# Kernel tuning notes

Measured on AMD Instinct MI355X. Metric: run time of the kernel, lower is better.

The kernel has to match this reference:

```python
import jax, jax.numpy as jnp
import numpy as np

N_NODES = 10000
N_EDGES = 320000
N_GRAPHS = 64


def _gcn_conv(x, edge_index, W, b, n):
    # PyG GCNConv: add self-loops, symmetric deg^-1/2 normalization, x@W, scatter-add at target, + bias
    loop = jnp.arange(n)
    src = jnp.concatenate([edge_index[0], loop])
    dst = jnp.concatenate([edge_index[1], loop])
    deg = jax.ops.segment_sum(jnp.ones_like(dst, dtype=x.dtype), dst, num_segments=n)
    dinv = jnp.where(deg > 0, 1.0 / jnp.sqrt(jnp.maximum(deg, 1.0)), 0.0)
    norm = dinv[src] * dinv[dst]            # [E']
    h = x @ W                               # [N, out]
    out = jax.ops.segment_sum(h[src] * norm[:, None], dst, num_segments=n)
    return out + b


def _mean_pool(x, batch, g):
    s = jax.ops.segment_sum(x, batch, num_segments=g)
    cnt = jax.ops.segment_sum(jnp.ones((x.shape[0],), x.dtype), batch, num_segments=g)
    return s / jnp.maximum(cnt, 1.0)[:, None]


def setup_inputs() -> dict:
    key = jax.random.key(0)
    ks = jax.random.split(key, 20)
    x = jax.random.normal(ks[0], (N_NODES, 1), dtype=jnp.float32)
    edge_index = jax.random.randint(ks[1], (2, N_EDGES), 0, N_NODES, dtype=jnp.int64)
    batch = jnp.sort(jax.random.randint(ks[2], (N_NODES,), 0, N_GRAPHS, dtype=jnp.int64))

    def lin(k, fi, fo):
        k1, k2 = jax.random.split(k)
        lim = 1.0 / np.sqrt(fi)
        W = jax.random.uniform(k1, (fi, fo), jnp.float32, -lim, lim)
        b = jax.random.uniform(k2, (fo,), jnp.float32, -lim, lim)
        return W, b

    W1, b1 = lin(ks[3], 1, 256)
    W2, b2 = lin(ks[4], 256, 256)
    W3, b3 = lin(ks[5], 256, 128)
    W4, b4 = lin(ks[6], 128, 128)
    W5, b5 = lin(ks[7], 128, 64)
    W6, b6 = lin(ks[8], 64, 32)
    W7, b7 = lin(ks[9], 32, 1)
    return dict(x=x, edge_index=edge_index, batch=batch,
                W1=W1, b1=b1, W2=W2, b2=b2, W3=W3, b3=b3, W4=W4, b4=b4,
                W5=W5, b5=b5, W6=W6, b6=b6, W7=W7, b7=b7)


def reference(x, edge_index, batch, W1, b1, W2, b2, W3, b3, W4, b4, W5, b5, W6, b6, W7, b7):
    n = x.shape[0]
    h = jax.nn.relu(_gcn_conv(x, edge_index, W1, b1, n))
    h = jax.nn.relu(_gcn_conv(h, edge_index, W2, b2, n))
    g = _mean_pool(h, batch, N_GRAPHS)          # [G, 256]
    g = jax.nn.relu(g @ W3 + b3)
    g = jax.nn.relu(g @ W4 + b4)
    g = jax.nn.relu(g @ W5 + b5)
    g = jax.nn.relu(g @ W6 + b6)
    y = (g @ W7 + b7).reshape(-1)               # [G]
    return y
```

## Files before the change

### kernel.cpp

```cpp
#include <hip/hip_runtime.h>

#define N_NODES  10000
#define N_EDGES  320000
#define N_GRAPHS 64
#define F 256
#define NTILES (((N_NODES + 63) / 64) * 4)
#define EDGE_BLOCKS (N_EDGES / 256)


struct Params {
    const float* x; const int* esrc; const int* edst; const int* batch;
    const float *W1, *b1, *W2, *b2, *W3, *b3, *W4, *b4, *W5, *b5, *W6, *b6, *W7, *b7;
    float* y;
    unsigned* cnti; int* offs; int* cursor; float* dinv; float* q; int* gstart;
    int* csr; float2* sd; float* aggb; float* out2;
};

#define EDGE_TERM(t)                                      \
    acc.x += fmaxf(fmaf((t).x, w.x, bv.x), 0.f) * (t).y;  \
    acc.y += fmaxf(fmaf((t).x, w.y, bv.y), 0.f) * (t).y;  \
    acc.z += fmaxf(fmaf((t).x, w.z, bv.z), 0.f) * (t).y;  \
    acc.w += fmaxf(fmaf((t).x, w.w, bv.w), 0.f) * (t).y;

__global__ __launch_bounds__(256) void k_deg(Params p) {
    int e = blockIdx.x * 256 + threadIdx.x;
    atomicAdd(&p.cnti[p.edst[e]], 1u);
}

__global__ __launch_bounds__(256) void k_scan(Params p) {
    __shared__ unsigned part[256];
    __shared__ unsigned baseShared;
    const int tid = threadIdx.x;
    const int CH = 40;
    int lo = tid * CH, hi = lo + CH;
    if (hi > N_NODES) hi = N_NODES;
    if (lo > N_NODES) lo = N_NODES;
    unsigned sum = 0;
    for (int i = lo; i < hi; i++) sum += p.cnti[i];
    part[tid] = sum;
    __syncthreads();
    for (int off = 1; off < 256; off <<= 1) {
        unsigned v = (tid >= off) ? part[tid - off] : 0u;
        __syncthreads();
        if (tid >= off) part[tid] += v;
        __syncthreads();
    }
    if (tid == 0)
        baseShared = (part[255] == (unsigned)N_EDGES) ? 0u : 0xAAAAAAAAu;
    __syncthreads();
    const unsigned B = baseShared;
    unsigned rawBase = (tid == 0) ? 0u : part[tid - 1];
    unsigned base = rawBase - (unsigned)lo * B;
    for (int i = lo; i < hi; i++) {
        unsigned c = p.cnti[i] - B;
        p.cnti[i] = c;
        p.offs[i] = (int)base; p.cursor[i] = (int)base; base += c;
        float di = 1.0f / sqrtf((float)(c + 1u));
        float xi = p.x[i];
        p.dinv[i] = di;
        p.q[i] = di * xi;
        p.sd[i] = make_float2(di * di * xi, di);
    }
    for (int i = lo; i < hi; i++) {
        int b = p.batch[i];
        if (i == 0) {
            for (int g = 0; g <= b; g++) p.gstart[g] = 0;
        } else {
            int bp = p.batch[i - 1];
            for (int g = bp + 1; g <= b; g++) p.gstart[g] = i;
        }
        if (i == N_NODES - 1) {
            for (int g = b + 1; g <= N_GRAPHS; g++) p.gstart[g] = N_NODES;
        }
    }
}

__global__ __launch_bounds__(256) void k_edge(Params p) {
    int e = blockIdx.x * 256 + threadIdx.x;
    int sv = p.esrc[e], dv = p.edst[e];
    int pos = atomicAdd(&p.cursor[dv], 1);
    p.csr[pos] = sv;
    atomicAdd(&p.sd[dv].x, p.dinv[dv] * p.q[sv]);
}

__global__ __launch_bounds__(256) void k_agg(Params p) {
    int wid  = (blockIdx.x * 256 + threadIdx.x) >> 6;
    int lane = threadIdx.x & 63;
    if (wid >= N_NODES) return;
    float4 w  = ((const float4*)p.W1)[lane];
    float4 bv = ((const float4*)p.b1)[lane];
    float2 self = p.sd[wid];
    float4 acc = {0.f, 0.f, 0.f, 0.f};
    EDGE_TERM(self)
    int lo = p.offs[wid], n = (int)p.cnti[wid];
    int j = 0;
    for (; j + 3 < n; j += 4) {
        int s0 = p.csr[lo + j],     s1 = p.csr[lo + j + 1];
        int s2 = p.csr[lo + j + 2], s3 = p.csr[lo + j + 3];
        float2 t0 = p.sd[s0], t1 = p.sd[s1], t2 = p.sd[s2], t3 = p.sd[s3];
        EDGE_TERM(t0) EDGE_TERM(t1) EDGE_TERM(t2) EDGE_TERM(t3)
    }
    for (; j < n; j++) {
        float2 t = p.sd[p.csr[lo + j]];
        EDGE_TERM(t)
    }
    float di = self.y;
    float4 o; o.x = acc.x * di; o.y = acc.y * di; o.z = acc.z * di; o.w = acc.w * di;
    ((float4*)(p.aggb + (size_t)wid * F))[lane] = o;
}

__global__ __launch_bounds__(256) void k_gemm(Params p) {
    __shared__ float As[16][68];
    __shared__ float Bs[16][64];
    const float* A = p.aggb;
    const float* B = p.W2;
    int tid  = threadIdx.x;
    int row0 = (blockIdx.x >> 2) * 64, col0 = (blockIdx.x & 3) * 64;
    int am = tid >> 2, ak = (tid & 3) * 4;
    int bk = tid >> 4, bn = (tid & 15) * 4;
    int ty = tid >> 4, tx = tid & 15;
    float acc[4][4] = {};
    for (int k0 = 0; k0 < 256; k0 += 16) {
        float4 av = {0.f, 0.f, 0.f, 0.f};
        if (row0 + am < N_NODES)
            av = *(const float4*)(A + (size_t)(row0 + am) * 256 + k0 + ak);
        As[ak + 0][am] = av.x; As[ak + 1][am] = av.y;
        As[ak + 2][am] = av.z; As[ak + 3][am] = av.w;
        float4 bvv = *(const float4*)(B + (size_t)(k0 + bk) * 256 + col0 + bn);
        *(float4*)&Bs[bk][bn] = bvv;
        __syncthreads();
        #pragma unroll
        for (int k = 0; k < 16; k++) {
            float4 a4 = *(const float4*)&As[k][ty * 4];
            float4 b4 = *(const float4*)&Bs[k][tx * 4];
            float a[4] = {a4.x, a4.y, a4.z, a4.w};
            float b[4] = {b4.x, b4.y, b4.z, b4.w};
            #pragma unroll
            for (int m = 0; m < 4; m++)
                #pragma unroll
                for (int n2 = 0; n2 < 4; n2++) acc[m][n2] += a[m] * b[n2];
        }
        __syncthreads();
    }
    #pragma unroll
    for (int m = 0; m < 4; m++) {
        int r = row0 + ty * 4 + m;
        if (r >= N_NODES) continue;
        #pragma unroll
        for (int n2 = 0; n2 < 4; n2++) {
            int c = col0 + tx * 4 + n2;
            p.out2[(size_t)r * 256 + c] = fmaxf(acc[m][n2] + p.b2[c], 0.0f);
        }
    }
}

__global__ __launch_bounds__(1024) void k_poolhead(Params p) {
    __shared__ float red[4][256];
    __shared__ float ha[256], hb[256];
    const int g = blockIdx.x;
    const int tid = threadIdx.x;
    const int col = tid & 255, rg = tid >> 8;
    int lo = p.gstart[g], hi = p.gstart[g + 1];
    float sum = 0.0f;
    for (int i = lo + rg; i < hi; i += 4)
        sum += p.out2[(size_t)i * F + col];
    red[rg][col] = sum;
    __syncthreads();
    if (tid < 256) {
        int len = hi - lo; if (len < 1) len = 1;
        ha[tid] = (red[0][tid] + red[1][tid] + red[2][tid] + red[3][tid]) / (float)len;
    }
    __syncthreads();
    if (tid < 128) { float acc = p.b3[tid]; for (int k = 0; k < 256; k++) acc += ha[k] * p.W3[k * 128 + tid]; hb[tid] = fmaxf(acc, 0.f); }
    __syncthreads();
    if (tid < 128) { float acc = p.b4[tid]; for (int k = 0; k < 128; k++) acc += hb[k] * p.W4[k * 128 + tid]; ha[tid] = fmaxf(acc, 0.f); }
    __syncthreads();
    if (tid < 64)  { float acc = p.b5[tid]; for (int k = 0; k < 128; k++) acc += ha[k] * p.W5[k * 64 + tid];  hb[tid] = fmaxf(acc, 0.f); }
    __syncthreads();
    if (tid < 32)  { float acc = p.b6[tid]; for (int k = 0; k < 64;  k++) acc += hb[k] * p.W6[k * 32 + tid];  ha[tid] = fmaxf(acc, 0.f); }
    __syncthreads();
    if (tid == 0)  { float acc = p.b7[0]; for (int k = 0; k < 32;  k++) acc += ha[k] * p.W7[k]; p.y[g] = acc; }
}

extern "C" void kernel_launch(void* const* d_in, const int* in_sizes, int n_in,
                              void* d_out, int out_size, void* d_ws, size_t ws_size,
                              hipStream_t stream) {
    Params P;
    P.x     = (const float*)d_in[0];
    P.esrc  = (const int*)d_in[1];
    P.edst  = ((const int*)d_in[1]) + N_EDGES;
    P.batch = (const int*)d_in[2];
    P.W1 = (const float*)d_in[3];  P.b1 = (const float*)d_in[4];
    P.W2 = (const float*)d_in[5];  P.b2 = (const float*)d_in[6];
    P.W3 = (const float*)d_in[7];  P.b3 = (const float*)d_in[8];
    P.W4 = (const float*)d_in[9];  P.b4 = (const float*)d_in[10];
    P.W5 = (const float*)d_in[11]; P.b5 = (const float*)d_in[12];
    P.W6 = (const float*)d_in[13]; P.b6 = (const float*)d_in[14];
    P.W7 = (const float*)d_in[15]; P.b7 = (const float*)d_in[16];
    P.y  = (float*)d_out;

    char* w = (char*)d_ws;
    size_t off = 0;
    auto alloc = [&](size_t bytes) { char* q = w + off; off += (bytes + 1023) & ~size_t(1023); return q; };
    P.cnti   = (unsigned*)alloc(N_NODES * 4);
    P.offs   = (int*)     alloc(N_NODES * 4);
    P.cursor = (int*)     alloc(N_NODES * 4);
    P.dinv   = (float*)   alloc(N_NODES * 4);
    P.q      = (float*)   alloc(N_NODES * 4);
    P.gstart = (int*)     alloc((N_GRAPHS + 1) * 4);
    P.csr    = (int*)     alloc(N_EDGES * 4);
    P.sd     = (float2*)  alloc((size_t)N_NODES * 8);
    P.aggb   = (float*)   alloc((size_t)N_NODES * F * 4);
    P.out2   = (float*)   alloc((size_t)N_NODES * F * 4);
    (void)ws_size; (void)in_sizes; (void)n_in; (void)out_size;

    hipLaunchKernelGGL(k_deg,      dim3(EDGE_BLOCKS), dim3(256),  0, stream, P);
    hipLaunchKernelGGL(k_scan,     dim3(1),           dim3(256),  0, stream, P);
    hipLaunchKernelGGL(k_edge,     dim3(EDGE_BLOCKS), dim3(256),  0, stream, P);
    hipLaunchKernelGGL(k_agg,      dim3((N_NODES * 64) / 256), dim3(256), 0, stream, P);
    hipLaunchKernelGGL(k_gemm,     dim3(NTILES),      dim3(256),  0, stream, P);
    hipLaunchKernelGGL(k_poolhead, dim3(N_GRAPHS),    dim3(1024), 0, stream, P);
}
```

Before: 289.8 us.

## Fuse layer-1 aggregation into layer-2 GEMM and widen the single-block scan

Merges the first-layer aggregation kernel and the second GEMM into one kernel. Each 512-thread block aggregates 32 node rows into shared memory and then multiplies them by W2, so the 10000x256 intermediate buffer is never written to or read back from global memory. The graph-start computation moves into the degree kernel, and the single-block scan goes from 256 to 1024 threads with counts cached in registers. The trade-off is heavier shared memory per block (about 69 KB), which lowers occupancy, and W2 is reloaded by all ~313 blocks.

```diff
diff --git a/kernel.cpp b/kernel.cpp
--- a/kernel.cpp
+++ b/kernel.cpp
@@ -4,8 +4,9 @@
 #define N_EDGES  320000
 #define N_GRAPHS 64
 #define F 256
-#define NTILES (((N_NODES + 63) / 64) * 4)
 #define EDGE_BLOCKS (N_EDGES / 256)
+#define AGG_ROWS 32
+#define AGG_BLOCKS ((N_NODES + AGG_ROWS - 1) / AGG_ROWS)
 
 
 struct Params {
@@ -13,7 +14,7 @@
     const float *W1, *b1, *W2, *b2, *W3, *b3, *W4, *b4, *W5, *b5, *W6, *b6, *W7, *b7;
     float* y;
     unsigned* cnti; int* offs; int* cursor; float* dinv; float* q; int* gstart;
-    int* csr; float2* sd; float* aggb; float* out2;
+    int* csr; float2* sd; float* out2;
 };
 
 #define EDGE_TERM(t)                                      \
@@ -23,36 +24,50 @@
     acc.w += fmaxf(fmaf((t).x, w.w, bv.w), 0.f) * (t).y;
 
 __global__ __launch_bounds__(256) void k_deg(Params p) {
-    int e = blockIdx.x * 256 + threadIdx.x;
-    atomicAdd(&p.cnti[p.edst[e]], 1u);
-}
-
-__global__ __launch_bounds__(256) void k_scan(Params p) {
-    __shared__ unsigned part[256];
+    int gid = blockIdx.x * 256 + threadIdx.x;
+    atomicAdd(&p.cnti[p.edst[gid]], 1u);
+    if (gid < N_NODES) {
+        int i = gid;
+        int b = p.batch[i];
+        if (i == 0) {
+            for (int g = 0; g <= b; g++) p.gstart[g] = 0;
+        } else {
+            int bp = p.batch[i - 1];
+            for (int g = bp + 1; g <= b; g++) p.gstart[g] = i;
+        }
+        if (i == N_NODES - 1) {
+            for (int g = b + 1; g <= N_GRAPHS; g++) p.gstart[g] = N_NODES;
+        }
+    }
+}
+
+__global__ __launch_bounds__(1024) void k_scan(Params p) {
+    __shared__ unsigned part[1024];
     __shared__ unsigned baseShared;
     const int tid = threadIdx.x;
-    const int CH = 40;
+    const int CH = 10;
     int lo = tid * CH, hi = lo + CH;
     if (hi > N_NODES) hi = N_NODES;
     if (lo > N_NODES) lo = N_NODES;
+    unsigned raw[10];
     unsigned sum = 0;
-    for (int i = lo; i < hi; i++) sum += p.cnti[i];
+    for (int i = lo; i < hi; i++) { raw[i - lo] = p.cnti[i]; sum += raw[i - lo]; }
     part[tid] = sum;
     __syncthreads();
-    for (int off = 1; off < 256; off <<= 1) {
+    for (int off = 1; off < 1024; off <<= 1) {
         unsigned v = (tid >= off) ? part[tid - off] : 0u;
         __syncthreads();
         if (tid >= off) part[tid] += v;
         __syncthreads();
     }
     if (tid == 0)
-        baseShared = (part[255] == (unsigned)N_EDGES) ? 0u : 0xAAAAAAAAu;
+        baseShared = (part[1023] == (unsigned)N_EDGES) ? 0u : 0xAAAAAAAAu;
     __syncthreads();
     const unsigned B = baseShared;
     unsigned rawBase = (tid == 0) ? 0u : part[tid - 1];
     unsigned base = rawBase - (unsigned)lo * B;
     for (int i = lo; i < hi; i++) {
-        unsigned c = p.cnti[i] - B;
+        unsigned c = raw[i - lo] - B;
         p.cnti[i] = c;
         p.offs[i] = (int)base; p.cursor[i] = (int)base; base += c;
         float di = 1.0f / sqrtf((float)(c + 1u));
@@ -61,18 +76,6 @@
         p.q[i] = di * xi;
         p.sd[i] = make_float2(di * di * xi, di);
     }
-    for (int i = lo; i < hi; i++) {
-        int b = p.batch[i];
-        if (i == 0) {
-            for (int g = 0; g <= b; g++) p.gstart[g] = 0;
-        } else {
-            int bp = p.batch[i - 1];
-            for (int g = bp + 1; g <= b; g++) p.gstart[g] = i;
-        }
-        if (i == N_NODES - 1) {
-            for (int g = b + 1; g <= N_GRAPHS; g++) p.gstart[g] = N_NODES;
-        }
-    }
 }
 
 __global__ __launch_bounds__(256) void k_edge(Params p) {
@@ -83,74 +86,79 @@
     atomicAdd(&p.sd[dv].x, p.dinv[dv] * p.q[sv]);
 }
 
-__global__ __launch_bounds__(256) void k_agg(Params p) {
-    int wid  = (blockIdx.x * 256 + threadIdx.x) >> 6;
-    int lane = threadIdx.x & 63;
-    if (wid >= N_NODES) return;
-    float4 w  = ((const float4*)p.W1)[lane];
-    float4 bv = ((const float4*)p.b1)[lane];
-    float2 self = p.sd[wid];
-    float4 acc = {0.f, 0.f, 0.f, 0.f};
-    EDGE_TERM(self)
-    int lo = p.offs[wid], n = (int)p.cnti[wid];
-    int j = 0;
-    for (; j + 3 < n; j += 4) {
-        int s0 = p.csr[lo + j],     s1 = p.csr[lo + j + 1];
-        int s2 = p.csr[lo + j + 2], s3 = p.csr[lo + j + 3];
-        float2 t0 = p.sd[s0], t1 = p.sd[s1], t2 = p.sd[s2], t3 = p.sd[s3];
-        EDGE_TERM(t0) EDGE_TERM(t1) EDGE_TERM(t2) EDGE_TERM(t3)
-    }
-    for (; j < n; j++) {
-        float2 t = p.sd[p.csr[lo + j]];
-        EDGE_TERM(t)
-    }
-    float di = self.y;
-    float4 o; o.x = acc.x * di; o.y = acc.y * di; o.z = acc.z * di; o.w = acc.w * di;
-    ((float4*)(p.aggb + (size_t)wid * F))[lane] = o;
-}
-
-__global__ __launch_bounds__(256) void k_gemm(Params p) {
-    __shared__ float As[16][68];
-    __shared__ float Bs[16][64];
-    const float* A = p.aggb;
-    const float* B = p.W2;
-    int tid  = threadIdx.x;
-    int row0 = (blockIdx.x >> 2) * 64, col0 = (blockIdx.x & 3) * 64;
-    int am = tid >> 2, ak = (tid & 3) * 4;
-    int bk = tid >> 4, bn = (tid & 15) * 4;
-    int ty = tid >> 4, tx = tid & 15;
-    float acc[4][4] = {};
-    for (int k0 = 0; k0 < 256; k0 += 16) {
-        float4 av = {0.f, 0.f, 0.f, 0.f};
-        if (row0 + am < N_NODES)
-            av = *(const float4*)(A + (size_t)(row0 + am) * 256 + k0 + ak);
-        As[ak + 0][am] = av.x; As[ak + 1][am] = av.y;
-        As[ak + 2][am] = av.z; As[ak + 3][am] = av.w;
-        float4 bvv = *(const float4*)(B + (size_t)(k0 + bk) * 256 + col0 + bn);
-        *(float4*)&Bs[bk][bn] = bvv;
-        __syncthreads();
+__global__ __launch_bounds__(512) void k_agemm(Params p) {
+    __shared__ float At[256][AGG_ROWS + 4];
+    __shared__ float Bs[32][256];
+    const int tid  = threadIdx.x;
+    const int wv   = tid >> 6;
+    const int lane = tid & 63;
+    const int row0 = blockIdx.x * AGG_ROWS;
+
+    {
+        float4 w  = ((const float4*)p.W1)[lane];
+        float4 bv = ((const float4*)p.b1)[lane];
         #pragma unroll
-        for (int k = 0; k < 16; k++) {
-            float4 a4 = *(const float4*)&As[k][ty * 4];
-            float4 b4 = *(const float4*)&Bs[k][tx * 4];
-            float a[4] = {a4.x, a4.y, a4.z, a4.w};
-            float b[4] = {b4.x, b4.y, b4.z, b4.w};
-            #pragma unroll
-            for (int m = 0; m < 4; m++)
-                #pragma unroll
-                for (int n2 = 0; n2 < 4; n2++) acc[m][n2] += a[m] * b[n2];
-        }
-        __syncthreads();
-    }
+        for (int m = 0; m < 4; m++) {
+            int r = wv * 4 + m;
+            int node = row0 + r;
+            float4 acc = {0.f, 0.f, 0.f, 0.f};
+            if (node < N_NODES) {
+                float2 self = p.sd[node];
+                EDGE_TERM(self)
+                int lo = p.offs[node], n = (int)p.cnti[node];
+                int j = 0;
+                for (; j + 3 < n; j += 4) {
+                    int s0 = p.csr[lo + j],     s1 = p.csr[lo + j + 1];
+                    int s2 = p.csr[lo + j + 2], s3 = p.csr[lo + j + 3];
+                    float2 t0 = p.sd[s0], t1 = p.sd[s1], t2 = p.sd[s2], t3 = p.sd[s3];
+                    EDGE_TERM(t0) EDGE_TERM(t1) EDGE_TERM(t2) EDGE_TERM(t3)
+                }
+                for (; j < n; j++) {
+                    float2 t = p.sd[p.csr[lo + j]];
+                    EDGE_TERM(t)
+                }
+                float di = self.y;
+                acc.x *= di; acc.y *= di; acc.z *= di; acc.w *= di;
+            }
+            At[lane * 4 + 0][r] = acc.x;
+            At[lane * 4 + 1][r] = acc.y;
+            At[lane * 4 + 2][r] = acc.z;
+            At[lane * 4 + 3][r] = acc.w;
+        }
+    }
+    __syncthreads();
+
+    float o[4][4] = {};
+    for (int k0 = 0; k0 < 256; k0 += 32) {
+        int bk = tid >> 4;
+        int bc = (tid & 15) * 4;
+        #pragma unroll
+        for (int qq = 0; qq < 4; qq++)
+            *(float4*)&Bs[bk][bc + qq * 64] =
+                *(const float4*)(p.W2 + (size_t)(k0 + bk) * 256 + bc + qq * 64);
+        __syncthreads();
+        #pragma unroll
+        for (int k = 0; k < 32; k++) {
+            float4 a = *(const float4*)&At[k0 + k][wv * 4];
+            float4 b = *(const float4*)&Bs[k][lane * 4];
+            o[0][0] += a.x * b.x; o[0][1] += a.x * b.y; o[0][2] += a.x * b.z; o[0][3] += a.x * b.w;
+            o[1][0] += a.y * b.x; o[1][1] += a.y * b.y; o[1][2] += a.y * b.z; o[1][3] += a.y * b.w;
+            o[2][0] += a.z * b.x; o[2][1] += a.z * b.y; o[2][2] += a.z * b.z; o[2][3] += a.z * b.w;
+            o[3][0] += a.w * b.x; o[3][1] += a.w * b.y; o[3][2] += a.w * b.z; o[3][3] += a.w * b.w;
+        }
+        __syncthreads();
+    }
+    float4 b2v = ((const float4*)p.b2)[lane];
     #pragma unroll
     for (int m = 0; m < 4; m++) {
-        int r = row0 + ty * 4 + m;
+        int r = row0 + wv * 4 + m;
         if (r >= N_NODES) continue;
-        #pragma unroll
-        for (int n2 = 0; n2 < 4; n2++) {
-            int c = col0 + tx * 4 + n2;
-            p.out2[(size_t)r * 256 + c] = fmaxf(acc[m][n2] + p.b2[c], 0.0f);
-        }
+        float4 res;
+        res.x = fmaxf(o[m][0] + b2v.x, 0.f);
+        res.y = fmaxf(o[m][1] + b2v.y, 0.f);
+        res.z = fmaxf(o[m][2] + b2v.z, 0.f);
+        res.w = fmaxf(o[m][3] + b2v.w, 0.f);
+        *(float4*)(p.out2 + (size_t)r * F + lane * 4) = res;
     }
 }
 
@@ -201,7 +209,7 @@
 
     char* w = (char*)d_ws;
     size_t off = 0;
-    auto alloc = [&](size_t bytes) { char* q = w + off; off += (bytes + 1023) & ~size_t(1023); return q; };
+    auto alloc = [&](size_t bytes) { char* r = w + off; off += (bytes + 1023) & ~size_t(1023); return r; };
     P.cnti   = (unsigned*)alloc(N_NODES * 4);
     P.offs   = (int*)     alloc(N_NODES * 4);
     P.cursor = (int*)     alloc(N_NODES * 4);
@@ -210,14 +218,12 @@
     P.gstart = (int*)     alloc((N_GRAPHS + 1) * 4);
     P.csr    = (int*)     alloc(N_EDGES * 4);
     P.sd     = (float2*)  alloc((size_t)N_NODES * 8);
-    P.aggb   = (float*)   alloc((size_t)N_NODES * F * 4);
     P.out2   = (float*)   alloc((size_t)N_NODES * F * 4);
     (void)ws_size; (void)in_sizes; (void)n_in; (void)out_size;
 
     hipLaunchKernelGGL(k_deg,      dim3(EDGE_BLOCKS), dim3(256),  0, stream, P);
-    hipLaunchKernelGGL(k_scan,     dim3(1),           dim3(256),  0, stream, P);
+    hipLaunchKernelGGL(k_scan,     dim3(1),           dim3(1024), 0, stream, P);
     hipLaunchKernelGGL(k_edge,     dim3(EDGE_BLOCKS), dim3(256),  0, stream, P);
-    hipLaunchKernelGGL(k_agg,      dim3((N_NODES * 64) / 256), dim3(256), 0, stream, P);
-    hipLaunchKernelGGL(k_gemm,     dim3(NTILES),      dim3(256),  0, stream, P);
+    hipLaunchKernelGGL(k_agemm,    dim3(AGG_BLOCKS),  dim3(512),  0, stream, P);
     hipLaunchKernelGGL(k_poolhead, dim3(N_GRAPHS),    dim3(1024), 0, stream, P);
 }
```

Measured after the change: 255.5 us. -11.9%, faster.
